# Performance work log

Measured on AMD Instinct MI355X. Metric: run time of the kernel, lower is better.

Reference implementation:

```python
import jax, jax.numpy as jnp
import numpy as np

TOPK = 2  # config.topk_exp


def setup_inputs() -> dict:
    key = jax.random.key(0)
    ks = jax.random.split(key, 4)
    B, S, D, F, E = 4, 1024, 768, 3072, 8
    scale_in = 1.0 / np.sqrt(D)
    scale_hid = 1.0 / np.sqrt(F)
    return {
        "x": jax.random.normal(ks[0], (B, S, D), dtype=jnp.float32),
        "router_w": jax.random.normal(ks[1], (E, D), dtype=jnp.float32) * scale_in,
        "w_fc": jax.random.normal(ks[2], (E, D, F), dtype=jnp.float32) * scale_in,
        "b_fc": jnp.zeros((E, F), dtype=jnp.float32),
        "w_proj": jax.random.normal(ks[3], (E, F, D), dtype=jnp.float32) * scale_hid,
        "b_proj": jnp.zeros((E, D), dtype=jnp.float32),
    }


def _moe_forward(x, router_w, w_fc, b_fc, w_proj, b_proj):
    B, S, D = x.shape
    E = router_w.shape[0]
    xt = x.reshape(-1, D)  # [T, D] tokens
    # per-token router: Linear(D, E, bias=False)
    gate_logits = xt @ router_w.T  # [T, E]
    # topk_exp > 1: raw logits -> topk -> softmax over the k selected logits
    weights, selected = jax.lax.top_k(gate_logits, TOPK)  # [T, k]
    weights = jax.nn.softmax(weights.astype(jnp.float32), axis=1).astype(x.dtype)
    # combine weights per expert: w[t, e] = sum_k weights[t,k] * (selected[t,k]==e)
    onehot = jax.nn.one_hot(selected, E, dtype=x.dtype)  # [T, k, E]
    comb = jnp.einsum('tk,tke->te', weights, onehot)  # [T, E]
    # expert MLP (GPT-2 style: fc -> gelu -> proj), evaluated densely then combined
    h = jax.nn.gelu(jnp.einsum('td,edf->etf', xt, w_fc) + b_fc[:, None, :], approximate=False)
    y = jnp.einsum('etf,efd->etd', h, w_proj) + b_proj[:, None, :]  # [E, T, D]
    out = jnp.einsum('te,etd->td', comb, y)  # weighted scatter-combine
    return out.reshape(B, S, D)


def reference(x, router_w, w_fc, b_fc, w_proj, b_proj):
    return _moe_forward(x, router_w, w_fc, b_fc, w_proj, b_proj)
```

## Files before the change

kernel.cpp:

```cpp
#include <hip/hip_runtime.h>
#include <hip/hip_bf16.h>

#define TT 4096
#define DD 768
#define FF 3072
#define EE 8
#define NSLOT 8192
#define NSLOT_PAD 8320

#define WVM4  0x0F74
#define WVM0  0x0F70

typedef __attribute__((ext_vector_type(8))) short bf16x8;
typedef __attribute__((ext_vector_type(4))) float f32x4;
typedef const __attribute__((address_space(1))) void* gas1_t;
typedef __attribute__((address_space(3))) void* las3_t;

__global__ __launch_bounds__(256) void router2_kernel(const float* __restrict__ x,
    const float* __restrict__ rw, int* __restrict__ tokE, float* __restrict__ tokW,
    int* __restrict__ blkCnt) {
  __shared__ float rws[EE * 832];
  __shared__ int cnt_s[EE];
  int tid = threadIdx.x;
  if (tid < EE) cnt_s[tid] = 0;
#pragma unroll
  for (int k = 0; k < 6; ++k) {
    int c = tid + k * 256;
    int e = c / 192, rem = c % 192;
    int s = rem / 12, i = rem % 12;
    float4 v = *(const float4*)&rw[e * DD + s * 48 + i * 4];
    *(float4*)&rws[e * 832 + s * 52 + i * 4] = v;
  }
  __syncthreads();
  int lane = tid & 63;
  int sl = lane & 15;
  int t = blockIdx.x * 16 + (tid >> 6) * 4 + (lane >> 4);
  const float4* xp = (const float4*)(x + (size_t)t * DD + sl * 48);
  float acc[EE];
#pragma unroll
  for (int e = 0; e < EE; ++e) acc[e] = 0.f;
#pragma unroll
  for (int i = 0; i < 12; ++i) {
    float4 xv = xp[i];
#pragma unroll
    for (int e = 0; e < EE; ++e) {
      float4 rv = *(const float4*)&rws[e * 832 + sl * 52 + i * 4];
      acc[e] = fmaf(xv.x, rv.x, fmaf(xv.y, rv.y, fmaf(xv.z, rv.z, fmaf(xv.w, rv.w, acc[e]))));
    }
  }
#pragma unroll
  for (int off = 8; off > 0; off >>= 1) {
#pragma unroll
    for (int e = 0; e < EE; ++e) acc[e] += __shfl_xor(acc[e], off);
  }
  if (sl == 0) {
    float v0 = -1e30f; int e0 = 0;
#pragma unroll
    for (int e = 0; e < EE; ++e) { if (acc[e] > v0) { v0 = acc[e]; e0 = e; } }
    float v1 = -1e30f; int e1 = 0;
#pragma unroll
    for (int e = 0; e < EE; ++e) { if (e != e0 && acc[e] > v1) { v1 = acc[e]; e1 = e; } }
    float w1 = 1.f / (1.f + __expf(v0 - v1));
    float w0 = 1.f - w1;
    tokE[2 * t] = e0; tokE[2 * t + 1] = e1;
    tokW[2 * t] = w0; tokW[2 * t + 1] = w1;
    atomicAdd(&cnt_s[e0], 1);
    atomicAdd(&cnt_s[e1], 1);
  }
  __syncthreads();
  if (tid < EE) blkCnt[blockIdx.x * EE + tid] = cnt_s[tid];
}

__global__ __launch_bounds__(256) void offsets2_kernel(const int* __restrict__ blkCnt,
    int* __restrict__ offs, int* __restrict__ blkBase,
    int* __restrict__ tile1, int* __restrict__ tile2, int* __restrict__ meta) {
  __shared__ int wsum[4][EE];
  int tid = threadIdx.x;
  int lane = tid & 63, w = tid >> 6;
  int c[EE], s[EE];
#pragma unroll
  for (int e = 0; e < EE; ++e) { c[e] = blkCnt[tid * EE + e]; s[e] = c[e]; }
#pragma unroll
  for (int off = 1; off < 64; off <<= 1) {
#pragma unroll
    for (int e = 0; e < EE; ++e) {
      int v = __shfl_up(s[e], off);
      if (lane >= off) s[e] += v;
    }
  }
  if (lane == 63) {
#pragma unroll
    for (int e = 0; e < EE; ++e) wsum[w][e] = s[e];
  }
  __syncthreads();
#pragma unroll
  for (int e = 0; e < EE; ++e) {
    int pre = 0;
    for (int w2 = 0; w2 < w; ++w2) pre += wsum[w2][e];
    s[e] += pre;
  }
  int tot[EE];
#pragma unroll
  for (int e = 0; e < EE; ++e) tot[e] = wsum[0][e] + wsum[1][e] + wsum[2][e] + wsum[3][e];
  int offl[EE + 1];
  offl[0] = 0;
#pragma unroll
  for (int e = 0; e < EE; ++e) offl[e + 1] = offl[e] + tot[e];
#pragma unroll
  for (int e = 0; e < EE; ++e) blkBase[tid * EE + e] = offl[e] + s[e] - c[e];
  if (tid == 0) {
    for (int e = 0; e <= EE; ++e) offs[e] = offl[e];
    int n1 = 0, n2 = 0;
    for (int e = 0; e < EE; ++e) { n1 += (tot[e] + 127) / 128; n2 += (tot[e] + 63) / 64; }
    meta[0] = n1; meta[1] = n2;
  }
  if (tid < EE) {
    int p1 = 0, p2 = 0;
    for (int e = 0; e < tid; ++e) { p1 += (tot[e] + 127) / 128; p2 += (tot[e] + 63) / 64; }
    for (int m = 0; m < tot[tid]; m += 128) tile1[p1++] = (tid << 20) | m;
    for (int m = 0; m < tot[tid]; m += 64)  tile2[p2++] = (tid << 20) | m;
  }
}

__global__ __launch_bounds__(256) void scatter_gather2_kernel(const float* __restrict__ x,
    const int* __restrict__ tokE, const float* __restrict__ tokW,
    const int* __restrict__ blkBase, int* __restrict__ slotIdx, float* __restrict__ slotW,
    int* __restrict__ slotTok, __hip_bfloat16* __restrict__ Xg) {
  __shared__ int base_s[EE], lcur[EE];
  __shared__ int sl_s[16][2];
  int tid = threadIdx.x;
  int b = blockIdx.x;
  if (tid < EE) { base_s[tid] = blkBase[b * EE + tid]; lcur[tid] = 0; }
  __syncthreads();
  if (tid < 16) {
    int t = b * 16 + tid;
    int e0 = tokE[2 * t], e1 = tokE[2 * t + 1];
    int s0 = base_s[e0] + atomicAdd(&lcur[e0], 1);
    int s1 = base_s[e1] + atomicAdd(&lcur[e1], 1);
    slotIdx[2 * t] = s0; slotIdx[2 * t + 1] = s1;
    slotW[s0] = tokW[2 * t]; slotW[s1] = tokW[2 * t + 1];
    slotTok[s0] = t; slotTok[s1] = t;
    sl_s[tid][0] = s0; sl_s[tid][1] = s1;
  }
  __syncthreads();
  int k = tid >> 4, p = tid & 15;
  int t = b * 16 + k;
  int s0 = sl_s[k][0], s1 = sl_s[k][1];
  const float4* src = (const float4*)(x + (size_t)t * DD);
  ushort4* d0 = (ushort4*)(Xg + (size_t)s0 * DD);
  ushort4* d1 = (ushort4*)(Xg + (size_t)s1 * DD);
#pragma unroll
  for (int i = 0; i < 12; ++i) {
    int idx = i * 16 + p;
    float4 v = src[idx];
    union { ushort4 u; __hip_bfloat16 h[4]; } cv;
    cv.h[0] = __float2bfloat16(v.x);
    cv.h[1] = __float2bfloat16(v.y);
    cv.h[2] = __float2bfloat16(v.z);
    cv.h[3] = __float2bfloat16(v.w);
    d0[idx] = cv.u;
    d1[idx] = cv.u;
  }
}

__global__ void transpose_convert_kernel(const float* __restrict__ w_fc, __hip_bfloat16* __restrict__ wfcT,
                                         const float* __restrict__ w_proj, __hip_bfloat16* __restrict__ wprojT) {
  __shared__ float tile[64][65];
  int bx = blockIdx.x;
  const float* S; __hip_bfloat16* D; int K, N, n0, k0;
  if (bx < 576) { S = w_fc;   D = wfcT;   K = DD; N = FF; n0 = (bx % 48) * 64; k0 = (bx / 48) * 64; }
  else { bx -= 576; S = w_proj; D = wprojT; K = FF; N = DD; n0 = (bx % 12) * 64; k0 = (bx / 12) * 64; }
  S += (size_t)blockIdx.z * K * N;
  D += (size_t)blockIdx.z * K * N;
  int tid = threadIdx.x;
#pragma unroll
  for (int i = 0; i < 4; ++i) {
    int slot = i * 256 + tid;
    int r = slot >> 4, c4 = slot & 15;
    float4 v = *(const float4*)&S[(size_t)(k0 + r) * N + n0 + c4 * 4];
    tile[r][c4 * 4 + 0] = v.x; tile[r][c4 * 4 + 1] = v.y;
    tile[r][c4 * 4 + 2] = v.z; tile[r][c4 * 4 + 3] = v.w;
  }
  __syncthreads();
#pragma unroll
  for (int i = 0; i < 4; ++i) {
    int slot = i * 256 + tid;
    int n = slot >> 4, kc = slot & 15;
    union { ushort4 u; __hip_bfloat16 h[4]; } cv;
    cv.h[0] = __float2bfloat16(tile[kc * 4 + 0][n]);
    cv.h[1] = __float2bfloat16(tile[kc * 4 + 1][n]);
    cv.h[2] = __float2bfloat16(tile[kc * 4 + 2][n]);
    cv.h[3] = __float2bfloat16(tile[kc * 4 + 3][n]);
    *(ushort4*)&D[(size_t)(n0 + n) * K + k0 + kc * 4] = cv.u;
  }
}

__device__ __forceinline__ float gelu_f(float v) {
  float z = v * 0.70710678118654752f;
  float az = fabsf(z);
  float t = 1.0f / (1.0f + 0.3275911f * az);
  float poly = t * (0.254829592f + t * (-0.284496736f + t * (1.421413741f +
               t * (-1.453152027f + t * 1.061405429f))));
  float erf_abs = 1.0f - poly * __expf(-az * az);
  float erf = copysignf(erf_abs, z);
  return 0.5f * v * (1.0f + erf);
}

__device__ __forceinline__ int swz4(int m) { return (m + (m >> 2)) & 3; }

#define G_ISSUE(PRE) \
  __builtin_amdgcn_global_load_lds((gas1_t)gA0, (las3_t)(&As[PRE][0] + fs0 * 8), 16, 0, 0); \
  __builtin_amdgcn_global_load_lds((gas1_t)gA1, (las3_t)(&As[PRE][0] + fs1 * 8), 16, 0, 0); \
  __builtin_amdgcn_global_load_lds((gas1_t)gB0, (las3_t)(&Bs[PRE][0] + fs0 * 8), 16, 0, 0); \
  __builtin_amdgcn_global_load_lds((gas1_t)gB1, (las3_t)(&Bs[PRE][0] + fs1 * 8), 16, 0, 0); \
  gA0 += 32; gA1 += 32; gB0 += 32; gB1 += 32;

#define G_COMP(CUR) \
  { const short* curA = &As[CUR][0]; const short* curB = &Bs[CUR][0]; \
    bf16x8 af[4], bfr[4]; \
    _Pragma("unroll") for (int mi = 0; mi < 4; ++mi) af[mi] = *(const bf16x8*)(curA + aoff[mi]); \
    _Pragma("unroll") for (int ni = 0; ni < 4; ++ni) bfr[ni] = *(const bf16x8*)(curB + boff[ni]); \
    _Pragma("unroll") for (int mi = 0; mi < 4; ++mi) \
      _Pragma("unroll") for (int ni = 0; ni < 4; ++ni) \
        acc[mi][ni] = __builtin_amdgcn_mfma_f32_16x16x32_bf16(af[mi], bfr[ni], acc[mi][ni], 0, 0, 0); }

#define S_MAIN(CUR, PRE) \
  __builtin_amdgcn_s_waitcnt(WVM4); \
  __builtin_amdgcn_s_barrier(); \
  G_ISSUE(PRE) \
  G_COMP(CUR)

#define S_TAIL(CUR, WAITIMM) \
  __builtin_amdgcn_s_waitcnt(WAITIMM); \
  __builtin_amdgcn_s_barrier(); \
  G_COMP(CUR)

__global__ __launch_bounds__(256) void gemm1_kernel(const __hip_bfloat16* __restrict__ Xg,
    const __hip_bfloat16* __restrict__ wfcT, const float* __restrict__ b_fc,
    __hip_bfloat16* __restrict__ H, const int* __restrict__ offs,
    const int* __restrict__ tile1, const int* __restrict__ meta) {
  __shared__ __align__(16) short As[3][128 * 32];
  __shared__ __align__(16) short Bs[3][128 * 32];
  int wg = blockIdx.x + 24 * blockIdx.y;
  int wl = (wg & 7) * 216 + (wg >> 3);
  int bx = wl % 24;
  int by = wl / 24;
  if (by >= meta[0]) return;
  int tv = tile1[by];
  int e = tv >> 20;
  int m_base = tv & 0xFFFFF;
  int off_e = offs[e];
  int n_e = offs[e + 1] - off_e;
  int n0 = bx * 128;
  const short* A = (const short*)Xg + (size_t)(off_e + m_base) * DD;
  const short* B = (const short*)wfcT + (size_t)e * FF * DD + (size_t)n0 * DD;
  int tid = threadIdx.x;
  int lane = tid & 63, wid = tid >> 6;
  int l15 = lane & 15, q = lane >> 4;
  int wm = wid & 1, wn = wid >> 1;
  int fs0 = tid, fs1 = tid + 256;
  int m0 = fs0 >> 2, c0 = (fs0 & 3) ^ swz4(m0);
  int m1 = fs1 >> 2, c1 = (fs1 & 3) ^ swz4(m1);
  const short* gA0 = A + (size_t)m0 * DD + c0 * 8;
  const short* gA1 = A + (size_t)m1 * DD + c1 * 8;
  const short* gB0 = B + (size_t)m0 * DD + c0 * 8;
  const short* gB1 = B + (size_t)m1 * DD + c1 * 8;
  int aoff[4], boff[4];
#pragma unroll
  for (int mi = 0; mi < 4; ++mi) {
    int r = wm * 64 + mi * 16 + l15;
    aoff[mi] = (r * 4 + (q ^ swz4(r))) * 8;
  }
#pragma unroll
  for (int ni = 0; ni < 4; ++ni) {
    int r = wn * 64 + ni * 16 + l15;
    boff[ni] = (r * 4 + (q ^ swz4(r))) * 8;
  }
  f32x4 acc[4][4] = {};
  G_ISSUE(0)
  G_ISSUE(1)
  for (int g = 0; g < 7; ++g) {
    S_MAIN(0, 2)
    S_MAIN(1, 0)
    S_MAIN(2, 1)
  }
  S_MAIN(0, 2)
  S_TAIL(1, WVM4)
  S_TAIL(2, WVM0)
  float bias[4];
#pragma unroll
  for (int ni = 0; ni < 4; ++ni) bias[ni] = b_fc[e * FF + n0 + wn * 64 + ni * 16 + l15];
  __hip_bfloat16* Hp = H + (size_t)(off_e + m_base) * FF + n0;
#pragma unroll
  for (int mi = 0; mi < 4; ++mi) {
#pragma unroll
    for (int r = 0; r < 4; ++r) {
      int ml = wm * 64 + mi * 16 + q * 4 + r;
      if (m_base + ml < n_e) {
#pragma unroll
        for (int ni = 0; ni < 4; ++ni) {
          int nl = wn * 64 + ni * 16 + l15;
          float v = acc[mi][ni][r] + bias[ni];
          Hp[(size_t)ml * FF + nl] = __float2bfloat16(gelu_f(v));
        }
      }
    }
  }
}

__global__ __launch_bounds__(256) void gemm2_kernel(const __hip_bfloat16* __restrict__ H,
    const __hip_bfloat16* __restrict__ wprojT, const float* __restrict__ b_proj,
    const float* __restrict__ slotW, const int* __restrict__ slotTok,
    float* __restrict__ out, const int* __restrict__ offs,
    const int* __restrict__ tile1, const int* __restrict__ meta) {
  __shared__ __align__(16) short As[3][128 * 32];
  __shared__ __align__(16) short Bs[3][128 * 32];
  int wg = blockIdx.x + 6 * blockIdx.y + 432 * blockIdx.z;
  int wl = (wg & 7) * 108 + (wg >> 3);
  int bx = wl % 6;
  int rest = wl / 6;
  int by = rest % 72;
  int kz = wl / 432;
  if (by >= meta[0]) return;
  int tv = tile1[by];
  int e = tv >> 20;
  int m_base = tv & 0xFFFFF;
  int off_e = offs[e];
  int n_e = offs[e + 1] - off_e;
  int n0 = bx * 128;
  const short* A = (const short*)H + (size_t)(off_e + m_base) * FF + kz * (FF / 2);
  const short* B = (const short*)wprojT + (size_t)e * DD * FF + (size_t)n0 * FF + kz * (FF / 2);
  int tid = threadIdx.x;
  int lane = tid & 63, wid = tid >> 6;
  int l15 = lane & 15, q = lane >> 4;
  int wm = wid & 1, wn = wid >> 1;
  int fs0 = tid, fs1 = tid + 256;
  int m0 = fs0 >> 2, c0 = (fs0 & 3) ^ swz4(m0);
  int m1 = fs1 >> 2, c1 = (fs1 & 3) ^ swz4(m1);
  const short* gA0 = A + (size_t)m0 * FF + c0 * 8;
  const short* gA1 = A + (size_t)m1 * FF + c1 * 8;
  const short* gB0 = B + (size_t)m0 * FF + c0 * 8;
  const short* gB1 = B + (size_t)m1 * FF + c1 * 8;
  int aoff[4], boff[4];
#pragma unroll
  for (int mi = 0; mi < 4; ++mi) {
    int r = wm * 64 + mi * 16 + l15;
    aoff[mi] = (r * 4 + (q ^ swz4(r))) * 8;
  }
#pragma unroll
  for (int ni = 0; ni < 4; ++ni) {
    int r = wn * 64 + ni * 16 + l15;
    boff[ni] = (r * 4 + (q ^ swz4(r))) * 8;
  }
  f32x4 acc[4][4] = {};
  G_ISSUE(0)
  G_ISSUE(1)
  for (int g = 0; g < 15; ++g) {
    S_MAIN(0, 2)
    S_MAIN(1, 0)
    S_MAIN(2, 1)
  }
  S_MAIN(0, 2)
  S_TAIL(1, WVM4)
  S_TAIL(2, WVM0)
  float bias[4];
#pragma unroll
  for (int ni = 0; ni < 4; ++ni)
    bias[ni] = (kz == 0) ? b_proj[e * DD + n0 + wn * 64 + ni * 16 + l15] : 0.f;
#pragma unroll
  for (int mi = 0; mi < 4; ++mi) {
#pragma unroll
    for (int r = 0; r < 4; ++r) {
      int ml = wm * 64 + mi * 16 + q * 4 + r;
      if (m_base + ml < n_e) {
        int slot = off_e + m_base + ml;
        float w = slotW[slot];
        int tok = slotTok[slot];
        float* op = out + (size_t)tok * DD + n0 + wn * 64;
#pragma unroll
        for (int ni = 0; ni < 4; ++ni)
          atomicAdd(&op[ni * 16 + l15], w * (acc[mi][ni][r] + bias[ni]));
      }
    }
  }
}

extern "C" void kernel_launch(void* const* d_in, const int* in_sizes, int n_in,
                              void* d_out, int out_size, void* d_ws, size_t ws_size,
                              hipStream_t stream) {
  const float* x        = (const float*)d_in[0];
  const float* router_w = (const float*)d_in[1];
  const float* w_fc     = (const float*)d_in[2];
  const float* b_fc     = (const float*)d_in[3];
  const float* w_proj   = (const float*)d_in[4];
  const float* b_proj   = (const float*)d_in[5];
  float* out = (float*)d_out;

  char* p = (char*)d_ws;
  auto alloc = [&](size_t bytes) {
    char* r = p;
    p += (bytes + 255) & ~(size_t)255;
    return r;
  };
  __hip_bfloat16* wfcT   = (__hip_bfloat16*)alloc((size_t)EE * FF * DD * 2);
  __hip_bfloat16* wprojT = (__hip_bfloat16*)alloc((size_t)EE * DD * FF * 2);
  __hip_bfloat16* Xg     = (__hip_bfloat16*)alloc((size_t)NSLOT_PAD * DD * 2);
  __hip_bfloat16* H      = (__hip_bfloat16*)alloc((size_t)NSLOT_PAD * FF * 2);
  int*   tokE    = (int*)alloc(TT * 2 * 4);
  float* tokW    = (float*)alloc(TT * 2 * 4);
  int*   slotIdx = (int*)alloc(TT * 2 * 4);
  float* slotW   = (float*)alloc(NSLOT_PAD * 4);
  int*   slotTok = (int*)alloc(NSLOT_PAD * 4);
  int*   blkCnt  = (int*)alloc(256 * EE * 4);
  int*   blkBase = (int*)alloc(256 * EE * 4);
  int*   tile1   = (int*)alloc(128 * 4);
  int*   tile2   = (int*)alloc(256 * 4);
  int*   offs    = (int*)alloc(64);
  int*   meta    = (int*)alloc(64);

  hipMemsetAsync(out, 0, (size_t)out_size * 4, stream);
  router2_kernel<<<256, 256, 0, stream>>>(x, router_w, tokE, tokW, blkCnt);
  offsets2_kernel<<<1, 256, 0, stream>>>(blkCnt, offs, blkBase, tile1, tile2, meta);
  scatter_gather2_kernel<<<256, 256, 0, stream>>>(x, tokE, tokW, blkBase, slotIdx, slotW, slotTok, Xg);
  transpose_convert_kernel<<<dim3(1152, 1, EE), 256, 0, stream>>>(w_fc, wfcT, w_proj, wprojT);
  gemm1_kernel<<<dim3(24, 72), 256, 0, stream>>>(Xg, wfcT, b_fc, H, offs, tile1, meta);
  gemm2_kernel<<<dim3(6, 72, 2), 256, 0, stream>>>(H, wprojT, b_proj, slotW, slotTok, out, offs, tile1, meta);
}
```

Baseline: 392.4 us.

## Switch GEMMs to BK=64 double buffering and drop gemm2 split-K

Both grouped GEMMs now load 128x64 K-tiles into a two-stage LDS buffer, replacing the three-stage 128x32 buffer, with an 8-way XOR swizzle. Each stage waits for all outstanding loads before its barrier. gemm2 no longer splits K in two, which halves its atomic adds into the output but halves the grid (432 blocks) and doubles the per-block K loop. Fewer barriers per K are traded for less load/compute overlap and lower parallelism in gemm2.

New measurement: 353.6 us. 9.9% less time.

```diff
diff --git a/kernel.cpp b/kernel.cpp
--- a/kernel.cpp
+++ b/kernel.cpp
@@ -8,7 +8,6 @@
 #define NSLOT 8192
 #define NSLOT_PAD 8320
 
-#define WVM4  0x0F74
 #define WVM0  0x0F70
 
 typedef __attribute__((ext_vector_type(8))) short bf16x8;
@@ -206,41 +205,67 @@
   return 0.5f * v * (1.0f + erf);
 }
 
-__device__ __forceinline__ int swz4(int m) { return (m + (m >> 2)) & 3; }
-
-#define G_ISSUE(PRE) \
-  __builtin_amdgcn_global_load_lds((gas1_t)gA0, (las3_t)(&As[PRE][0] + fs0 * 8), 16, 0, 0); \
-  __builtin_amdgcn_global_load_lds((gas1_t)gA1, (las3_t)(&As[PRE][0] + fs1 * 8), 16, 0, 0); \
-  __builtin_amdgcn_global_load_lds((gas1_t)gB0, (las3_t)(&Bs[PRE][0] + fs0 * 8), 16, 0, 0); \
-  __builtin_amdgcn_global_load_lds((gas1_t)gB1, (las3_t)(&Bs[PRE][0] + fs1 * 8), 16, 0, 0); \
-  gA0 += 32; gA1 += 32; gB0 += 32; gB1 += 32;
+#define G_ISSUE(NXT) \
+  _Pragma("unroll") for (int i = 0; i < 4; ++i) { \
+    __builtin_amdgcn_global_load_lds((gas1_t)gA[i], (las3_t)(&As[NXT][0] + fsd[i]), 16, 0, 0); \
+    __builtin_amdgcn_global_load_lds((gas1_t)gB[i], (las3_t)(&Bs[NXT][0] + fsd[i]), 16, 0, 0); \
+    gA[i] += 64; gB[i] += 64; }
 
 #define G_COMP(CUR) \
-  { const short* curA = &As[CUR][0]; const short* curB = &Bs[CUR][0]; \
-    bf16x8 af[4], bfr[4]; \
-    _Pragma("unroll") for (int mi = 0; mi < 4; ++mi) af[mi] = *(const bf16x8*)(curA + aoff[mi]); \
-    _Pragma("unroll") for (int ni = 0; ni < 4; ++ni) bfr[ni] = *(const bf16x8*)(curB + boff[ni]); \
-    _Pragma("unroll") for (int mi = 0; mi < 4; ++mi) \
-      _Pragma("unroll") for (int ni = 0; ni < 4; ++ni) \
-        acc[mi][ni] = __builtin_amdgcn_mfma_f32_16x16x32_bf16(af[mi], bfr[ni], acc[mi][ni], 0, 0, 0); }
-
-#define S_MAIN(CUR, PRE) \
-  __builtin_amdgcn_s_waitcnt(WVM4); \
+  { const short* cA = &As[CUR][0]; const short* cB = &Bs[CUR][0]; \
+    _Pragma("unroll") for (int s = 0; s < 2; ++s) { \
+      bf16x8 af[4], bfr[4]; \
+      _Pragma("unroll") for (int mi = 0; mi < 4; ++mi) af[mi] = *(const bf16x8*)(cA + aoff[mi][s]); \
+      _Pragma("unroll") for (int ni = 0; ni < 4; ++ni) bfr[ni] = *(const bf16x8*)(cB + boff[ni][s]); \
+      _Pragma("unroll") for (int mi = 0; mi < 4; ++mi) \
+        _Pragma("unroll") for (int ni = 0; ni < 4; ++ni) \
+          acc[mi][ni] = __builtin_amdgcn_mfma_f32_16x16x32_bf16(af[mi], bfr[ni], acc[mi][ni], 0, 0, 0); } }
+
+#define S_MAIN(CUR, NXT) \
+  __builtin_amdgcn_s_waitcnt(WVM0); \
   __builtin_amdgcn_s_barrier(); \
-  G_ISSUE(PRE) \
+  G_ISSUE(NXT) \
   G_COMP(CUR)
 
-#define S_TAIL(CUR, WAITIMM) \
-  __builtin_amdgcn_s_waitcnt(WAITIMM); \
+#define S_LAST(CUR) \
+  __builtin_amdgcn_s_waitcnt(WVM0); \
   __builtin_amdgcn_s_barrier(); \
   G_COMP(CUR)
+
+#define GEMM_SETUP(STRIDE) \
+  int tid = threadIdx.x; \
+  int lane = tid & 63, wid = tid >> 6; \
+  int l15 = lane & 15, q = lane >> 4; \
+  int wm = wid & 1, wn = wid >> 1; \
+  int fsd[4]; \
+  const short* gA[4]; \
+  const short* gB[4]; \
+  _Pragma("unroll") for (int i = 0; i < 4; ++i) { \
+    int fs = tid + i * 256; \
+    int m = fs >> 3, c = (fs & 7) ^ (m & 7); \
+    fsd[i] = fs * 8; \
+    gA[i] = A + (size_t)m * STRIDE + c * 8; \
+    gB[i] = B + (size_t)m * STRIDE + c * 8; \
+  } \
+  int aoff[4][2], boff[4][2]; \
+  _Pragma("unroll") for (int mi = 0; mi < 4; ++mi) { \
+    int r = wm * 64 + mi * 16 + l15; \
+    _Pragma("unroll") for (int s = 0; s < 2; ++s) \
+      aoff[mi][s] = r * 64 + ((((s << 2) | q) ^ (r & 7)) * 8); \
+  } \
+  _Pragma("unroll") for (int ni = 0; ni < 4; ++ni) { \
+    int r = wn * 64 + ni * 16 + l15; \
+    _Pragma("unroll") for (int s = 0; s < 2; ++s) \
+      boff[ni][s] = r * 64 + ((((s << 2) | q) ^ (r & 7)) * 8); \
+  } \
+  f32x4 acc[4][4] = {};
 
 __global__ __launch_bounds__(256) void gemm1_kernel(const __hip_bfloat16* __restrict__ Xg,
     const __hip_bfloat16* __restrict__ wfcT, const float* __restrict__ b_fc,
     __hip_bfloat16* __restrict__ H, const int* __restrict__ offs,
     const int* __restrict__ tile1, const int* __restrict__ meta) {
-  __shared__ __align__(16) short As[3][128 * 32];
-  __shared__ __align__(16) short Bs[3][128 * 32];
+  __shared__ __align__(16) short As[2][128 * 64];
+  __shared__ __align__(16) short Bs[2][128 * 64];
   int wg = blockIdx.x + 24 * blockIdx.y;
   int wl = (wg & 7) * 216 + (wg >> 3);
   int bx = wl % 24;
@@ -254,39 +279,14 @@
   int n0 = bx * 128;
   const short* A = (const short*)Xg + (size_t)(off_e + m_base) * DD;
   const short* B = (const short*)wfcT + (size_t)e * FF * DD + (size_t)n0 * DD;
-  int tid = threadIdx.x;
-  int lane = tid & 63, wid = tid >> 6;
-  int l15 = lane & 15, q = lane >> 4;
-  int wm = wid & 1, wn = wid >> 1;
-  int fs0 = tid, fs1 = tid + 256;
-  int m0 = fs0 >> 2, c0 = (fs0 & 3) ^ swz4(m0);
-  int m1 = fs1 >> 2, c1 = (fs1 & 3) ^ swz4(m1);
-  const short* gA0 = A + (size_t)m0 * DD + c0 * 8;
-  const short* gA1 = A + (size_t)m1 * DD + c1 * 8;
-  const short* gB0 = B + (size_t)m0 * DD + c0 * 8;
-  const short* gB1 = B + (size_t)m1 * DD + c1 * 8;
-  int aoff[4], boff[4];
-#pragma unroll
-  for (int mi = 0; mi < 4; ++mi) {
-    int r = wm * 64 + mi * 16 + l15;
-    aoff[mi] = (r * 4 + (q ^ swz4(r))) * 8;
-  }
-#pragma unroll
-  for (int ni = 0; ni < 4; ++ni) {
-    int r = wn * 64 + ni * 16 + l15;
-    boff[ni] = (r * 4 + (q ^ swz4(r))) * 8;
-  }
-  f32x4 acc[4][4] = {};
+  GEMM_SETUP(DD)
   G_ISSUE(0)
-  G_ISSUE(1)
-  for (int g = 0; g < 7; ++g) {
-    S_MAIN(0, 2)
+  for (int g = 0; g < 5; ++g) {
+    S_MAIN(0, 1)
     S_MAIN(1, 0)
-    S_MAIN(2, 1)
-  }
-  S_MAIN(0, 2)
-  S_TAIL(1, WVM4)
-  S_TAIL(2, WVM0)
+  }
+  S_MAIN(0, 1)
+  S_LAST(1)
   float bias[4];
 #pragma unroll
   for (int ni = 0; ni < 4; ++ni) bias[ni] = b_fc[e * FF + n0 + wn * 64 + ni * 16 + l15];
@@ -313,14 +313,12 @@
     const float* __restrict__ slotW, const int* __restrict__ slotTok,
     float* __restrict__ out, const int* __restrict__ offs,
     const int* __restrict__ tile1, const int* __restrict__ meta) {
-  __shared__ __align__(16) short As[3][128 * 32];
-  __shared__ __align__(16) short Bs[3][128 * 32];
-  int wg = blockIdx.x + 6 * blockIdx.y + 432 * blockIdx.z;
-  int wl = (wg & 7) * 108 + (wg >> 3);
+  __shared__ __align__(16) short As[2][128 * 64];
+  __shared__ __align__(16) short Bs[2][128 * 64];
+  int wg = blockIdx.x + 6 * blockIdx.y;
+  int wl = (wg & 7) * 54 + (wg >> 3);
   int bx = wl % 6;
-  int rest = wl / 6;
-  int by = rest % 72;
-  int kz = wl / 432;
+  int by = wl / 6;
   if (by >= meta[0]) return;
   int tv = tile1[by];
   int e = tv >> 20;
@@ -328,45 +326,20 @@
   int off_e = offs[e];
   int n_e = offs[e + 1] - off_e;
   int n0 = bx * 128;
-  const short* A = (const short*)H + (size_t)(off_e + m_base) * FF + kz * (FF / 2);
-  const short* B = (const short*)wprojT + (size_t)e * DD * FF + (size_t)n0 * FF + kz * (FF / 2);
-  int tid = threadIdx.x;
-  int lane = tid & 63, wid = tid >> 6;
-  int l15 = lane & 15, q = lane >> 4;
-  int wm = wid & 1, wn = wid >> 1;
-  int fs0 = tid, fs1 = tid + 256;
-  int m0 = fs0 >> 2, c0 = (fs0 & 3) ^ swz4(m0);
-  int m1 = fs1 >> 2, c1 = (fs1 & 3) ^ swz4(m1);
-  const short* gA0 = A + (size_t)m0 * FF + c0 * 8;
-  const short* gA1 = A + (size_t)m1 * FF + c1 * 8;
-  const short* gB0 = B + (size_t)m0 * FF + c0 * 8;
-  const short* gB1 = B + (size_t)m1 * FF + c1 * 8;
-  int aoff[4], boff[4];
-#pragma unroll
-  for (int mi = 0; mi < 4; ++mi) {
-    int r = wm * 64 + mi * 16 + l15;
-    aoff[mi] = (r * 4 + (q ^ swz4(r))) * 8;
-  }
-#pragma unroll
-  for (int ni = 0; ni < 4; ++ni) {
-    int r = wn * 64 + ni * 16 + l15;
-    boff[ni] = (r * 4 + (q ^ swz4(r))) * 8;
-  }
-  f32x4 acc[4][4] = {};
+  const short* A = (const short*)H + (size_t)(off_e + m_base) * FF;
+  const short* B = (const short*)wprojT + (size_t)e * DD * FF + (size_t)n0 * FF;
+  GEMM_SETUP(FF)
   G_ISSUE(0)
-  G_ISSUE(1)
-  for (int g = 0; g < 15; ++g) {
-    S_MAIN(0, 2)
+  for (int g = 0; g < 23; ++g) {
+    S_MAIN(0, 1)
     S_MAIN(1, 0)
-    S_MAIN(2, 1)
-  }
-  S_MAIN(0, 2)
-  S_TAIL(1, WVM4)
-  S_TAIL(2, WVM0)
+  }
+  S_MAIN(0, 1)
+  S_LAST(1)
   float bias[4];
 #pragma unroll
   for (int ni = 0; ni < 4; ++ni)
-    bias[ni] = (kz == 0) ? b_proj[e * DD + n0 + wn * 64 + ni * 16 + l15] : 0.f;
+    bias[ni] = b_proj[e * DD + n0 + wn * 64 + ni * 16 + l15];
 #pragma unroll
   for (int mi = 0; mi < 4; ++mi) {
 #pragma unroll
@@ -424,5 +397,5 @@
   scatter_gather2_kernel<<<256, 256, 0, stream>>>(x, tokE, tokW, blkBase, slotIdx, slotW, slotTok, Xg);
   transpose_convert_kernel<<<dim3(1152, 1, EE), 256, 0, stream>>>(w_fc, wfcT, w_proj, wprojT);
   gemm1_kernel<<<dim3(24, 72), 256, 0, stream>>>(Xg, wfcT, b_fc, H, offs, tile1, meta);
-  gemm2_kernel<<<dim3(6, 72, 2), 256, 0, stream>>>(H, wprojT, b_proj, slotW, slotTok, out, offs, tile1, meta);
-}
+  gemm2_kernel<<<dim3(6, 72), 256, 0, stream>>>(H, wprojT, b_proj, slotW, slotTok, out, offs, tile1, meta);
+}
```
